# Kernel optimization log

Measured on AMD Instinct MI355X. Metric: run time of the kernel, lower is better.

Reference implementation:

```python
import jax, jax.numpy as jnp
import numpy as np

B = 128            # number of subgraphs (one head, one tail each)
NODES_PER_G = 64
N = B * NODES_PER_G  # 8192 total nodes
E = 131072           # total edges in the batched graph
NUM_RELS = 200
D = 64               # rel_emb_dim
EMB = 64             # emb_dim
L = 3                # num_gcn_layers (jumping-knowledge concat)
REPR = L * EMB       # 192, g.ndata['repr'] feature width
LINK_MODE = 6


def setup_inputs() -> dict:
    key = jax.random.key(0)
    ks = jax.random.split(key, 10)
    node_repr = jax.random.normal(ks[0], (N, REPR), jnp.float32)
    edge_src = jax.random.randint(ks[1], (E,), 0, N, dtype=jnp.int32)
    edge_dst = jax.random.randint(ks[2], (E,), 0, N, dtype=jnp.int32)
    edge_type = jax.random.randint(ks[3], (E,), 0, NUM_RELS, dtype=jnp.int32)
    rel_labels = jax.random.randint(ks[4], (B,), 0, NUM_RELS, dtype=jnp.int32)
    node_graph_id = (jnp.arange(N) // NODES_PER_G).astype(jnp.int32)
    head_ids = (jnp.arange(B) * NODES_PER_G).astype(jnp.int32)   # node with id==1 per graph
    tail_ids = head_ids + 1                                      # node with id==2 per graph
    rel_emb_w = jax.random.normal(ks[5], (NUM_RELS, D), jnp.float32)
    W_reld = jax.random.normal(ks[6], (LINK_MODE, D, D), jnp.float32) * 0.05
    b_reld = jnp.zeros((LINK_MODE, D), jnp.float32)
    Wc = jax.random.normal(ks[7], (D, 2 * D), jnp.float32) * 0.05
    bc = jnp.zeros((D,), jnp.float32)
    Wf = jax.random.normal(ks[8], (1, 3 * REPR + D), jnp.float32) * 0.05
    bf = jnp.zeros((1,), jnp.float32)
    return {
        'node_repr': node_repr, 'rel_emb_w': rel_emb_w, 'W_reld': W_reld,
        'b_reld': b_reld, 'Wc': Wc, 'bc': bc, 'Wf': Wf, 'bf': bf,
        'edge_src': edge_src, 'edge_dst': edge_dst, 'edge_type': edge_type,
        'rel_labels': rel_labels, 'node_graph_id': node_graph_id,
        'head_ids': head_ids, 'tail_ids': tail_ids,
    }


def reference(node_repr, rel_emb_w, W_reld, b_reld, Wc, bc, Wf, bf,
              edge_src, edge_dst, edge_type, rel_labels, node_graph_id,
              head_ids, tail_ids):
    f32 = jnp.float32
    nb = head_ids.shape[0]
    # Six edge connection modes, [B, E] each (row b selects edges incident to
    # the head/tail node of subgraph b).
    io = (edge_dst[None, :] == head_ids[:, None]).astype(f32)  # in_edge_out
    oo = (edge_src[None, :] == head_ids[:, None]).astype(f32)  # out_edge_out
    ii = (edge_dst[None, :] == tail_ids[:, None]).astype(f32)  # in_edge_in
    oi = (edge_src[None, :] == tail_ids[:, None]).astype(f32)  # out_edge_in
    m5 = oo * ii   # edge_mode_5: head -> tail edges
    m6 = io * oi   # edge_mode_6: tail -> head edges
    modes = jnp.stack([io - m6, oo - m5, ii - m5, oi - m6, m5, m6])  # [6,B,E]
    norms = modes.sum(-1, keepdims=True) + 1e-30                      # [6,B,1]
    # Per-mode linear transform of relation embeddings, then aggregate.
    rel_feat = rel_emb_w[edge_type]                                   # [E,D]
    trans = jnp.einsum('ed,mfd->mef', rel_feat, W_reld) + b_reld[:, None, :]  # [6,E,D]
    contrib = jnp.einsum('mbe,med->mbd', modes, trans) / norms        # [6,B,D]
    rel_neighbor = contrib.mean(0)                                    # sum(...)/link_mode
    rel_final = jnp.concatenate([rel_neighbor, rel_emb_w[rel_labels]], -1) @ Wc.T + bc
    rel_final = jax.nn.relu(rel_final)
    rel_final = rel_final / jnp.maximum(
        jnp.linalg.norm(rel_final, axis=-1, keepdims=True), 1e-12)
    # mean_nodes(g, 'repr') per subgraph
    g_sum = jax.ops.segment_sum(node_repr, node_graph_id, num_segments=nb)
    counts = jax.ops.segment_sum(jnp.ones((node_repr.shape[0],), f32),
                                 node_graph_id, num_segments=nb)
    g_out = g_sum / counts[:, None]
    g_rep = jnp.concatenate(
        [g_out, node_repr[head_ids], node_repr[tail_ids], rel_final], -1)
    return g_rep @ Wf.T + bf   # [B, 1]
```

## Files before the change

kernel.cpp:

```cpp
#include <hip/hip_runtime.h>

#define NGRAPH 128
#define NEDGE  131072
#define DIM    64
#define REPRW  192
#define NTHREADS 1024
#define MAXHITS 1024

__global__ __launch_bounds__(NTHREADS) void fused_graph_kernel(
    const float* __restrict__ node_repr, const float* __restrict__ rel_emb,
    const float* __restrict__ W_reld, const float* __restrict__ b_reld,
    const float* __restrict__ Wc, const float* __restrict__ bc,
    const float* __restrict__ Wf, const float* __restrict__ bf,
    const int* __restrict__ esrc, const int* __restrict__ edst,
    const int* __restrict__ etype, const int* __restrict__ rel_labels,
    const int* __restrict__ head_ids, const int* __restrict__ tail_ids,
    float* __restrict__ out)
{
    const int b    = blockIdx.x;
    const int tid  = threadIdx.x;
    const int base = b << 6;
    const int wave = tid >> 6;
    const int lane = tid & 63;

    __shared__ __align__(16) float shS[6 * 64];
    __shared__ float shCnt[6];
    __shared__ int   shList[MAXHITS];
    __shared__ int   shNHits;
    __shared__ float sh_grep[640];
    __shared__ float sh_part[4 * 192];
    __shared__ float sh_v[6 * 64];
    __shared__ float sh_rn[64];
    __shared__ float sh_Wc[64 * 129];
    __shared__ float sh_red[16];

    if (tid < 384) shS[tid] = 0.0f;
    if (tid < 6)   shCnt[tid] = 0.0f;
    if (tid == 0)  shNHits = 0;
    __syncthreads();

    {
        int r = tid / 192, col = tid - r * 192;
        if (tid < 768) {
            const float* p = node_repr + (size_t)(base + r * 16) * REPRW + col;
            float a = 0.0f;
            #pragma unroll
            for (int n = 0; n < 16; n++) a += p[(size_t)n * REPRW];
            sh_part[r * 192 + col] = a;
        }
        if (tid < 192) {
            sh_grep[192 + tid] = node_repr[(size_t)head_ids[b] * REPRW + tid];
            sh_grep[384 + tid] = node_repr[(size_t)tail_ids[b] * REPRW + tid];
        }
    }

    {
        const int4* s4 = (const int4*)esrc;
        const int4* d4 = (const int4*)edst;
        for (int i = tid; i < NEDGE / 4; i += NTHREADS) {
            int4 ss = s4[i];
            int4 dd = d4[i];
            #pragma unroll
            for (int c = 0; c < 4; c++) {
                int s = (c == 0) ? ss.x : (c == 1) ? ss.y : (c == 2) ? ss.z : ss.w;
                int d = (c == 0) ? dd.x : (c == 1) ? dd.y : (c == 2) ? dd.z : dd.w;
                bool hd = (unsigned)(d - base) < 2u;
                bool hs = (unsigned)(s - base) < 2u;
                if (hd | hs) {
                    int et = etype[4 * i + c];
                    if (hd) {
                        if (d == base) {
                            int m = (s == base + 1) ? 5 : 0;
                            int idx = atomicAdd(&shNHits, 1);
                            if (idx < MAXHITS) shList[idx] = (m << 16) | et;
                            atomicAdd(&shCnt[m], 1.0f);
                        } else if (s != base) {
                            int idx = atomicAdd(&shNHits, 1);
                            if (idx < MAXHITS) shList[idx] = (2 << 16) | et;
                            atomicAdd(&shCnt[2], 1.0f);
                        }
                    }
                    if (hs) {
                        if (s == base) {
                            int m = (d == base + 1) ? 4 : 1;
                            int idx = atomicAdd(&shNHits, 1);
                            if (idx < MAXHITS) shList[idx] = (m << 16) | et;
                            atomicAdd(&shCnt[m], 1.0f);
                        } else if (d != base) {
                            int idx = atomicAdd(&shNHits, 1);
                            if (idx < MAXHITS) shList[idx] = (3 << 16) | et;
                            atomicAdd(&shCnt[3], 1.0f);
                        }
                    }
                }
            }
        }
    }
    __syncthreads();

    {
        int nh = shNHits < MAXHITS ? shNHits : MAXHITS;
        for (int h = wave; h < nh; h += 16) {
            int ent = shList[h];
            int m = ent >> 16, t = ent & 0xffff;
            atomicAdd(&shS[m * 64 + lane], rel_emb[t * 64 + lane]);
        }
        if (tid < 192)
            sh_grep[tid] = (sh_part[tid] + sh_part[192 + tid] +
                            sh_part[384 + tid] + sh_part[576 + tid]) * (1.0f / 64.0f);
    }
    __syncthreads();

    if (tid < 384) {
        int m = wave, f = lane;
        const float4* Wrow = (const float4*)(W_reld + (m * 64 + f) * 64);
        const float4* Sv   = (const float4*)(shS + m * 64);
        float dot = 0.0f;
        #pragma unroll
        for (int k = 0; k < 16; k++) {
            float4 w = Wrow[k];
            float4 sv = Sv[k];
            dot += w.x * sv.x + w.y * sv.y + w.z * sv.z + w.w * sv.w;
        }
        float cm = shCnt[m];
        sh_v[m * 64 + f] = (dot + cm * b_reld[m * 64 + f]) / (cm + 1e-30f);
    } else {
        for (int j = tid - 384; j < 64 * 128; j += NTHREADS - 384) {
            int row = j >> 7, col = j & 127;
            sh_Wc[row * 129 + col] = Wc[j];
        }
    }
    __syncthreads();

    if (tid < 64) {
        sh_rn[tid] = (sh_v[tid] + sh_v[64 + tid] + sh_v[128 + tid] +
                      sh_v[192 + tid] + sh_v[256 + tid] + sh_v[320 + tid]) * (1.0f / 6.0f);
    }
    __syncthreads();

    if (tid < 64) {
        const float* rl = rel_emb + rel_labels[b] * DIM;
        const float* Wrow = sh_Wc + tid * 129;
        float z = bc[tid];
        #pragma unroll 8
        for (int j = 0; j < 64; j++) z += sh_rn[j] * Wrow[j];
        #pragma unroll 8
        for (int j = 0; j < 64; j++) z += rl[j] * Wrow[64 + j];
        z = fmaxf(z, 0.0f);
        float sq = z * z;
        #pragma unroll
        for (int off = 32; off >= 1; off >>= 1) sq += __shfl_xor(sq, off);
        float nrm = fmaxf(sqrtf(sq), 1e-12f);
        sh_grep[576 + tid] = z / nrm;
    }
    __syncthreads();

    if (tid < 640) {
        float p = sh_grep[tid] * Wf[tid];
        #pragma unroll
        for (int off = 32; off >= 1; off >>= 1) p += __shfl_xor(p, off);
        if (lane == 0) sh_red[wave] = p;
    }
    __syncthreads();
    if (tid == 0) {
        float acc = bf[0];
        #pragma unroll
        for (int w = 0; w < 10; w++) acc += sh_red[w];
        out[b] = acc;
    }
}

extern "C" void kernel_launch(void* const* d_in, const int* in_sizes, int n_in,
                              void* d_out, int out_size, void* d_ws, size_t ws_size,
                              hipStream_t stream) {
    (void)in_sizes; (void)n_in; (void)out_size; (void)d_ws; (void)ws_size;

    const float* node_repr = (const float*)d_in[0];
    const float* rel_emb   = (const float*)d_in[1];
    const float* W_reld    = (const float*)d_in[2];
    const float* b_reld    = (const float*)d_in[3];
    const float* Wc        = (const float*)d_in[4];
    const float* bc        = (const float*)d_in[5];
    const float* Wf        = (const float*)d_in[6];
    const float* bf        = (const float*)d_in[7];
    const int*   esrc      = (const int*)d_in[8];
    const int*   edst      = (const int*)d_in[9];
    const int*   etype     = (const int*)d_in[10];
    const int*   rel_labels= (const int*)d_in[11];
    const int*   head_ids  = (const int*)d_in[13];
    const int*   tail_ids  = (const int*)d_in[14];

    fused_graph_kernel<<<NGRAPH, NTHREADS, 0, stream>>>(
        node_repr, rel_emb, W_reld, b_reld, Wc, bc, Wf, bf,
        esrc, edst, etype, rel_labels, head_ids, tail_ids, (float*)d_out);
}
```

Before: 112.3 us.

## Scan edges once across grid with cooperative launch and global atomics

Before, each of the 128 blocks scanned all 131072 edges to find the ones touching its own head and tail nodes. Now the kernel runs as a cooperative launch: each thread reads exactly one edge, and the matching edges scatter per-mode sums and counts into a global workspace with atomics. Grid-wide syncs separate zeroing, scattering and the per-block finish. This removes the 128x redundant edge reads at the cost of two grid barriers, global atomic traffic, and a dependence on the edge count equalling grid size times block size.

```diff
diff --git a/kernel.cpp b/kernel.cpp
--- a/kernel.cpp
+++ b/kernel.cpp
@@ -1,13 +1,17 @@
 #include <hip/hip_runtime.h>
+#include <hip/hip_cooperative_groups.h>
+
+namespace cg = cooperative_groups;
 
 #define NGRAPH 128
 #define NEDGE  131072
 #define DIM    64
 #define REPRW  192
 #define NTHREADS 1024
-#define MAXHITS 1024
+#define NZ_S   (6 * NGRAPH * DIM)
+#define NZ_ALL (NZ_S + 6 * NGRAPH)
 
-__global__ __launch_bounds__(NTHREADS) void fused_graph_kernel(
+__global__ __launch_bounds__(NTHREADS) void coop_graph_kernel(
     const float* __restrict__ node_repr, const float* __restrict__ rel_emb,
     const float* __restrict__ W_reld, const float* __restrict__ b_reld,
     const float* __restrict__ Wc, const float* __restrict__ bc,
@@ -15,8 +19,10 @@
     const int* __restrict__ esrc, const int* __restrict__ edst,
     const int* __restrict__ etype, const int* __restrict__ rel_labels,
     const int* __restrict__ head_ids, const int* __restrict__ tail_ids,
+    float* __restrict__ S, float* __restrict__ cnt,
     float* __restrict__ out)
 {
+    cg::grid_group grid = cg::this_grid();
     const int b    = blockIdx.x;
     const int tid  = threadIdx.x;
     const int base = b << 6;
@@ -25,8 +31,6 @@
 
     __shared__ __align__(16) float shS[6 * 64];
     __shared__ float shCnt[6];
-    __shared__ int   shList[MAXHITS];
-    __shared__ int   shNHits;
     __shared__ float sh_grep[640];
     __shared__ float sh_part[4 * 192];
     __shared__ float sh_v[6 * 64];
@@ -34,80 +38,70 @@
     __shared__ float sh_Wc[64 * 129];
     __shared__ float sh_red[16];
 
-    if (tid < 384) shS[tid] = 0.0f;
-    if (tid < 6)   shCnt[tid] = 0.0f;
-    if (tid == 0)  shNHits = 0;
-    __syncthreads();
-
     {
-        int r = tid / 192, col = tid - r * 192;
+        int gz = b * NTHREADS + tid;
+        if (gz < NZ_S)          S[gz] = 0.0f;
+        else if (gz < NZ_ALL)   cnt[gz - NZ_S] = 0.0f;
+    }
+    {
         if (tid < 768) {
+            int r = tid / 192, col = tid - r * 192;
             const float* p = node_repr + (size_t)(base + r * 16) * REPRW + col;
             float a = 0.0f;
             #pragma unroll
             for (int n = 0; n < 16; n++) a += p[(size_t)n * REPRW];
             sh_part[r * 192 + col] = a;
-        }
-        if (tid < 192) {
-            sh_grep[192 + tid] = node_repr[(size_t)head_ids[b] * REPRW + tid];
-            sh_grep[384 + tid] = node_repr[(size_t)tail_ids[b] * REPRW + tid];
+        } else if (tid < 960) {
+            int j = tid - 768;
+            sh_grep[192 + j] = node_repr[(size_t)head_ids[b] * REPRW + j];
+            sh_grep[384 + j] = node_repr[(size_t)tail_ids[b] * REPRW + j];
         }
     }
+    grid.sync();
 
     {
-        const int4* s4 = (const int4*)esrc;
-        const int4* d4 = (const int4*)edst;
-        for (int i = tid; i < NEDGE / 4; i += NTHREADS) {
-            int4 ss = s4[i];
-            int4 dd = d4[i];
-            #pragma unroll
-            for (int c = 0; c < 4; c++) {
-                int s = (c == 0) ? ss.x : (c == 1) ? ss.y : (c == 2) ? ss.z : ss.w;
-                int d = (c == 0) ? dd.x : (c == 1) ? dd.y : (c == 2) ? dd.z : dd.w;
-                bool hd = (unsigned)(d - base) < 2u;
-                bool hs = (unsigned)(s - base) < 2u;
-                if (hd | hs) {
-                    int et = etype[4 * i + c];
-                    if (hd) {
-                        if (d == base) {
-                            int m = (s == base + 1) ? 5 : 0;
-                            int idx = atomicAdd(&shNHits, 1);
-                            if (idx < MAXHITS) shList[idx] = (m << 16) | et;
-                            atomicAdd(&shCnt[m], 1.0f);
-                        } else if (s != base) {
-                            int idx = atomicAdd(&shNHits, 1);
-                            if (idx < MAXHITS) shList[idx] = (2 << 16) | et;
-                            atomicAdd(&shCnt[2], 1.0f);
-                        }
-                    }
-                    if (hs) {
-                        if (s == base) {
-                            int m = (d == base + 1) ? 4 : 1;
-                            int idx = atomicAdd(&shNHits, 1);
-                            if (idx < MAXHITS) shList[idx] = (m << 16) | et;
-                            atomicAdd(&shCnt[m], 1.0f);
-                        } else if (d != base) {
-                            int idx = atomicAdd(&shNHits, 1);
-                            if (idx < MAXHITS) shList[idx] = (3 << 16) | et;
-                            atomicAdd(&shCnt[3], 1.0f);
-                        }
-                    }
-                }
-            }
+        int e = b * NTHREADS + tid;
+        int s  = esrc[e];
+        int d  = edst[e];
+        int et = etype[e];
+        int dl = d & 63, sl = s & 63;
+        int b_d = d >> 6, b_s = s >> 6;
+
+        int mode_d = -1;
+        if (dl == 0)      mode_d = (s == d + 1) ? 5 : 0;
+        else if (dl == 1) mode_d = (s == d - 1) ? -1 : 2;
+
+        int mode_s = -1;
+        if (sl == 0)      mode_s = (d == s + 1) ? 4 : 1;
+        else if (sl == 1) mode_s = (d == s - 1) ? -1 : 3;
+
+        unsigned long long mask = __ballot(mode_d >= 0);
+        while (mask) {
+            int l = __builtin_ctzll(mask); mask &= mask - 1;
+            int mm = __shfl(mode_d, l);
+            int bb = __shfl(b_d, l);
+            int tt = __shfl(et, l);
+            atomicAdd(&S[(mm * NGRAPH + bb) * DIM + lane], rel_emb[tt * DIM + lane]);
+            if (lane == 0) atomicAdd(&cnt[mm * NGRAPH + bb], 1.0f);
+        }
+        mask = __ballot(mode_s >= 0);
+        while (mask) {
+            int l = __builtin_ctzll(mask); mask &= mask - 1;
+            int mm = __shfl(mode_s, l);
+            int bb = __shfl(b_s, l);
+            int tt = __shfl(et, l);
+            atomicAdd(&S[(mm * NGRAPH + bb) * DIM + lane], rel_emb[tt * DIM + lane]);
+            if (lane == 0) atomicAdd(&cnt[mm * NGRAPH + bb], 1.0f);
         }
     }
-    __syncthreads();
+    grid.sync();
 
-    {
-        int nh = shNHits < MAXHITS ? shNHits : MAXHITS;
-        for (int h = wave; h < nh; h += 16) {
-            int ent = shList[h];
-            int m = ent >> 16, t = ent & 0xffff;
-            atomicAdd(&shS[m * 64 + lane], rel_emb[t * 64 + lane]);
-        }
-        if (tid < 192)
-            sh_grep[tid] = (sh_part[tid] + sh_part[192 + tid] +
-                            sh_part[384 + tid] + sh_part[576 + tid]) * (1.0f / 64.0f);
+    if (tid < 384)                    shS[tid] = S[((tid >> 6) * NGRAPH + b) * DIM + (tid & 63)];
+    else if (tid < 390)               shCnt[tid - 384] = cnt[(tid - 384) * NGRAPH + b];
+    else if (tid >= 512 && tid < 704) {
+        int j = tid - 512;
+        sh_grep[j] = (sh_part[j] + sh_part[192 + j] +
+                      sh_part[384 + j] + sh_part[576 + j]) * (1.0f / 64.0f);
     }
     __syncthreads();
 
@@ -173,7 +167,7 @@
 extern "C" void kernel_launch(void* const* d_in, const int* in_sizes, int n_in,
                               void* d_out, int out_size, void* d_ws, size_t ws_size,
                               hipStream_t stream) {
-    (void)in_sizes; (void)n_in; (void)out_size; (void)d_ws; (void)ws_size;
+    (void)in_sizes; (void)n_in; (void)out_size; (void)ws_size;
 
     const float* node_repr = (const float*)d_in[0];
     const float* rel_emb   = (const float*)d_in[1];
@@ -190,7 +184,16 @@
     const int*   head_ids  = (const int*)d_in[13];
     const int*   tail_ids  = (const int*)d_in[14];
 
-    fused_graph_kernel<<<NGRAPH, NTHREADS, 0, stream>>>(
-        node_repr, rel_emb, W_reld, b_reld, Wc, bc, Wf, bf,
-        esrc, edst, etype, rel_labels, head_ids, tail_ids, (float*)d_out);
+    float* S   = (float*)d_ws;
+    float* cnt = S + NZ_S;
+    float* outp = (float*)d_out;
+
+    void* args[] = {
+        (void*)&node_repr, (void*)&rel_emb, (void*)&W_reld, (void*)&b_reld,
+        (void*)&Wc, (void*)&bc, (void*)&Wf, (void*)&bf,
+        (void*)&esrc, (void*)&edst, (void*)&etype, (void*)&rel_labels,
+        (void*)&head_ids, (void*)&tail_ids, (void*)&S, (void*)&cnt, (void*)&outp
+    };
+    hipLaunchCooperativeKernel((void*)coop_graph_kernel, dim3(NGRAPH),
+                               dim3(NTHREADS), args, 0, stream);
 }
```

New measurement: 154.1 us. 1.37x slower.
